# Optimization experiments

Hardware: AMD Instinct MI355X
Metric: run time of the kernel (lower is better)

Reference implementation:

```python
import jax, jax.numpy as jnp
from jax import lax
import numpy as np

B, L, E, H, R, V = 64, 512, 256, 256, 50, 20000
NEG = 1e10  # seq_max_pool mask constant


def _conv1d(x, w, b):
    # x: (B, L, Cin) -> (B, L, Cout); kernel 3, 'same' padding (pad=1)
    y = lax.conv_general_dilated(x.transpose(0, 2, 1), w, (1,), [(1, 1)],
                                 dimension_numbers=('NCH', 'OIH', 'NCH'))
    return y.transpose(0, 2, 1) + b


def _lstm_step(x, h, c, W_ih, W_hh, b_ih, b_hh):
    # single-step LSTM, PyTorch gate order (i, f, g, o)
    gates = x @ W_ih.T + b_ih + h @ W_hh.T + b_hh
    i, f, g, o = jnp.split(gates, 4, axis=-1)
    c = jax.nn.sigmoid(f) * c + jax.nn.sigmoid(i) * jnp.tanh(g)
    h = jax.nn.sigmoid(o) * jnp.tanh(c)
    return h, c


def _attention(q, ctx, W_attn, b_attn):
    # Luong attention (IBM seq2seq style). q: (B,E), ctx: (B,L,E)
    scores = jnp.einsum('be,ble->bl', q, ctx)
    attn = jax.nn.softmax(scores, axis=-1)
    mix = jnp.einsum('bl,ble->be', attn, ctx)
    return jnp.tanh(jnp.concatenate([mix, q], axis=-1) @ W_attn.T + b_attn)


def setup_inputs() -> dict:
    key = jax.random.key(0)
    ks = jax.random.split(key, 25)
    s = 0.05
    return {
        'encoder_o': jax.random.normal(ks[0], (B, L, E), jnp.float32),
        'h0': jax.random.normal(ks[1], (B, H), jnp.float32),
        'c0': jax.random.normal(ks[2], (B, H), jnp.float32),
        'sos_emb': jax.random.normal(ks[3], (E,), jnp.float32) * s,
        'rel_emb': jax.random.normal(ks[4], (R, E), jnp.float32) * s,
        'W_ih': jax.random.normal(ks[5], (4 * H, E), jnp.float32) * s,
        'W_hh': jax.random.normal(ks[6], (4 * H, H), jnp.float32) * s,
        'b_ih': jax.random.normal(ks[7], (4 * H,), jnp.float32) * s,
        'b_hh': jax.random.normal(ks[8], (4 * H,), jnp.float32) * s,
        'W_attn': jax.random.normal(ks[9], (E, 2 * E), jnp.float32) * s,
        'b_attn': jax.random.normal(ks[10], (E,), jnp.float32) * s,
        'conv_rel_w': jax.random.normal(ks[11], (E, 2 * H, 3), jnp.float32) * s,
        'conv_rel_b': jax.random.normal(ks[12], (E,), jnp.float32) * s,
        'conv_ent_w': jax.random.normal(ks[13], (E, 2 * H, 3), jnp.float32) * s,
        'conv_ent_b': jax.random.normal(ks[14], (E,), jnp.float32) * s,
        'W_rel': jax.random.normal(ks[15], (R, E), jnp.float32) * s,
        'b_rel': jax.random.normal(ks[16], (R,), jnp.float32) * s,
        'w_e1': jax.random.normal(ks[17], (E,), jnp.float32) * s,
        'b_e1': jax.random.normal(ks[18], (1,), jnp.float32) * s,
        'w_e2': jax.random.normal(ks[19], (E,), jnp.float32) * s,
        'b_e2': jax.random.normal(ks[20], (1,), jnp.float32) * s,
        'T': jax.random.randint(ks[21], (B, L), 0, V),
        'R_in': jax.random.randint(ks[22], (B,), 0, R),
        'S_K1': jax.random.randint(ks[23], (B,), 0, L),
        'S_K2': jax.random.randint(ks[24], (B,), 0, L),
    }


def reference(encoder_o, h0, c0, sos_emb, rel_emb, W_ih, W_hh, b_ih, b_hh,
              W_attn, b_attn, conv_rel_w, conv_rel_b, conv_ent_w, conv_ent_b,
              W_rel, b_rel, w_e1, b_e1, w_e2, b_e2, T, R_in, S_K1, S_K2):
    # train_forward, order=('subject','predicate','object') -> sos2ent, ent2rel, rel2ent
    # dropout is identity (eval mode)
    mask = (T > 0).astype(encoder_o.dtype)[..., None]  # (B,L,1)
    bidx = jnp.arange(B)

    def step(inp, h, c, enc, conv_w, conv_b):
        # forward_step: one LSTM step + attention over enc
        h, c = _lstm_step(inp, h, c, W_ih, W_hh, b_ih, b_hh)
        out = _attention(h, enc, W_attn, b_attn)  # (B,E)
        # seq_and_vec + permute + conv1d + permute
        cat = jnp.concatenate([enc, jnp.broadcast_to(out[:, None, :], enc.shape)], axis=-1)
        new_enc = _conv1d(cat, conv_w, conv_b)  # (B,L,E)
        a = jax.nn.gelu(new_enc, approximate=False)
        return a, new_enc, h, c

    # step 1: sos -> entity heads
    a, enc1, h, c = step(jnp.broadcast_to(sos_emb, (B, E)), h0, c0, encoder_o,
                         conv_ent_w, conv_ent_b)
    t1e1 = a @ w_e1 + b_e1  # (B,L)
    t1e2 = a @ w_e2 + b_e2

    # step 2: gathered entity span vectors -> relation logits (masked max-pool)
    inp = enc1[bidx, S_K1] + enc1[bidx, S_K2]  # seq_gather + sum, (B,E)
    a, enc2, h, c = step(inp, h, c, enc1, conv_rel_w, conv_rel_b)
    logits = a @ W_rel.T + b_rel  # (B,L,R)
    t2rel = jnp.max(logits - (1.0 - mask) * NEG, axis=1)  # seq_max_pool -> (B,R)

    # step 3: relation embedding -> entity heads
    a, enc3, h, c = step(rel_emb[R_in], h, c, enc2, conv_ent_w, conv_ent_b)
    t3e1 = a @ w_e1 + b_e1
    t3e2 = a @ w_e2 + b_e2

    return (t1e1, t1e2, t2rel, t3e1, t3e2)
```

## Files before the change

kernel.cpp:

```cpp
#include <hip/hip_runtime.h>
#include <math.h>

#define B_ 64
#define L_ 512
#define E_ 256
#define H_ 256
#define R_ 50
#define NEG_ 1.0e10f

typedef __bf16 bf16x8 __attribute__((ext_vector_type(8)));
typedef float f32x4 __attribute__((ext_vector_type(4)));

__device__ __forceinline__ float sigmoidf_(float x) { return 1.0f / (1.0f + expf(-x)); }
__device__ __forceinline__ float geluf_(float x) { return 0.5f * x * (1.0f + erff(x * 0.7071067811865476f)); }
__device__ __forceinline__ unsigned short f2bf(float x) {
    unsigned u = __float_as_uint(x);
    return (unsigned short)((u + 0x7fffu + ((u >> 16) & 1u)) >> 16);
}
__device__ __forceinline__ float bf2f(unsigned u) { return __uint_as_float(u << 16); }

__global__ void k_packs(const float* __restrict__ encoder_o, unsigned short* __restrict__ encBF0,
                        const float* __restrict__ conv_ent_w, const float* __restrict__ conv_rel_w,
                        unsigned short* __restrict__ bpE, unsigned short* __restrict__ bpR,
                        const float* __restrict__ W_rel, unsigned short* __restrict__ wpR,
// ... 25 lines not shown
        int idx = (blk - 8384) * 256 + t;
        int l = idx & 63, kc = (idx >> 6) & 7, of = idx / (8 * 64);
        int r = of * 16 + (l & 15);
        int k = kc * 32 + ((l >> 4) << 3);
        unsigned short v[8];
#pragma unroll
        for (int j = 0; j < 8; ++j) v[j] = (r < R_) ? f2bf(W_rel[(size_t)r * E_ + k + j]) : 0;
        unsigned int* dst = (unsigned int*)&wpR[(size_t)idx * 8];
#pragma unroll
        for (int j = 0; j < 4; ++j) dst[j] = (unsigned int)v[2 * j] | ((unsigned int)v[2 * j + 1] << 16);
    } else if (blk < 8904) {
        const float* w = (blk < 8648) ? conv_ent_w : conv_rel_w;
        float* wpk = (blk < 8648) ? wpkE : wpkR;
        int idx = (blk - ((blk < 8648) ? 8392 : 8648)) * 256 + t;
        int o = idx >> 8, c = idx & 255;
        const float* p = &w[(size_t)o * 1536 + 768 + c * 3];
        float w0 = p[0], w1 = p[1], w2 = p[2];
        wpk[c * 256 + o] = w0;
        wpk[65536 + c * 256 + o] = w0 + w1 + w2;
        wpk[131072 + c * 256 + o] = w2;
    } else {
        int idx = (blk - 8904) * 256 + t;
        int o = idx >> 9, k = idx & 511;
        WTat[k * 256 + o] = W_attn[idx];
    }
}

template <int MODE>
__global__ __launch_bounds__(256) void k_lstm_gemm(
    const float* __restrict__ xsrc_f, const unsigned short* __restrict__ encg,
    const int* __restrict__ i1, const int* __restrict__ i2, const int* __restrict__ rin,
    const float* __restrict__ hprev,
    const float* __restrict__ W_ih, const float* __restrict__ W_hh,
    float* __restrict__ gates) {
    const int g0 = blockIdx.x * 64;
    const int half = blockIdx.y, z = blockIdx.z;
    const int t = threadIdx.x, tx = t & 15, ty = t >> 4;
    __shared__ float Xs[64][68];
    __shared__ float Wt[64][68];
    const float* Wsrc = half ? W_hh : W_ih;
    float acc[4][4] = {{0.f}};
    for (int kb = z * 128; kb < z * 128 + 128; kb += 64) {
        __syncthreads();
#pragma unroll
        for (int i = 0; i < 4; ++i) {
            int idx = i * 256 + t;
            int row = idx >> 4, kk = (idx & 15) << 2;
            float4 xv;
            if (half) {
                xv = *(const float4*)&hprev[row * 256 + kb + kk];
            } else if (MODE == 0) {
                xv = *(const float4*)&xsrc_f[kb + kk];
            } else if (MODE == 2) {
                xv = *(const float4*)&xsrc_f[(size_t)rin[row] * 256 + kb + kk];
            } else {
                const unsigned short* p1 = &encg[((size_t)row * L_ + i1[row]) * E_ + kb + kk];
                const unsigned short* p2 = &encg[((size_t)row * L_ + i2[row]) * E_ + kb + kk];
                uint2 a = *(const uint2*)p1, b2 = *(const uint2*)p2;
                xv.x = bf2f(a.x & 0xffffu) + bf2f(b2.x & 0xffffu);
                xv.y = bf2f(a.x >> 16) + bf2f(b2.x >> 16);
                xv.z = bf2f(a.y & 0xffffu) + bf2f(b2.y & 0xffffu);
                xv.w = bf2f(a.y >> 16) + bf2f(b2.y >> 16);
            }
            *(float4*)&Xs[row][kk] = xv;
            *(float4*)&Wt[row][kk] = *(const float4*)&Wsrc[(size_t)(g0 + row) * 256 + kb + kk];
        }
        __syncthreads();
#pragma unroll
        for (int kk = 0; kk < 64; kk += 4) {
            float4 xv[4], wv[4];
#pragma unroll
            for (int i = 0; i < 4; ++i) xv[i] = *(const float4*)&Xs[ty * 4 + i][kk];
#pragma unroll
            for (int j = 0; j < 4; ++j) wv[j] = *(const float4*)&Wt[tx * 4 + j][kk];
#pragma unroll
            for (int i = 0; i < 4; ++i)
#pragma unroll
                for (int j = 0; j < 4; ++j)
                    acc[i][j] += xv[i].x * wv[j].x + xv[i].y * wv[j].y + xv[i].z * wv[j].z + xv[i].w * wv[j].w;
        }
    }
    const int seg = half * 2 + z;
#pragma unroll
    for (int i = 0; i < 4; ++i)
#pragma unroll
        for (int j = 0; j < 4; ++j)
            gates[(size_t)seg * 65536 + (size_t)(ty * 4 + i) * 1024 + g0 + tx * 4 + j] = acc[i][j];
}

__global__ __launch_bounds__(256) void k_attn_part(
    const float* __restrict__ gates, const float* __restrict__ b_ih, const float* __restrict__ b_hh,
    const float* __restrict__ c_in, float* __restrict__ c_out, float* __restrict__ h_out,
    const unsigned short* __restrict__ encbf,
    float* __restrict__ mixp, float* __restrict__ stats) {
    int b = blockIdx.y, ch = blockIdx.x, t = threadIdx.x;
    __shared__ float hs[E_];
    __shared__ float scp[64][4];
    __shared__ float sc[64];
    {
        size_t ba = (size_t)b * 1024;
        float g4[4];
#pragma unroll
        for (int g = 0; g < 4; ++g) {
            float acc = b_ih[g * 256 + t] + b_hh[g * 256 + t];
#pragma unroll
            for (int seg = 0; seg < 4; ++seg) acc += gates[(size_t)seg * 65536 + ba + g * 256 + t];
            g4[g] = acc;
        }
        float c = sigmoidf_(g4[1]) * c_in[b * H_ + t] + sigmoidf_(g4[0]) * tanhf(g4[2]);
        float hv = sigmoidf_(g4[3]) * tanhf(c);
        hs[t] = hv;
        if (ch == 0) { h_out[b * H_ + t] = hv; c_out[b * H_ + t] = c; }
    }
    __syncthreads();
    {
        int row = t >> 2, es = t & 3;
        const uint4* p = (const uint4*)&encbf[((size_t)b * L_ + ch * 64 + row) * E_ + es * 64];
        float acc = 0.f;
#pragma unroll
        for (int k = 0; k < 8; ++k) {
// ... 70 lines not shown
#pragma unroll
        for (int k2 = 0; k2 < 16; ++k2) s += red[k2][oc2][j];
        int o = oc * 64 + t;
        aout[b * E_ + o] = tanhf(s + b_attn[o]);
    }
}

__global__ __launch_bounds__(256) void k_post2(
    const float* __restrict__ aout, const float* __restrict__ wpk,
    float* __restrict__ cr0, float* __restrict__ fullv, float* __restrict__ cr2) {
    int b = blockIdx.x, m = blockIdx.y, t = threadIdx.x;
    __shared__ float os[256];
    __shared__ float red[4][64][4];
    os[t] = aout[b * E_ + t];
    __syncthreads();
    int ocol = t & 63, cs = t >> 6;
    int o4 = ocol * 4;
    const float* wp = &wpk[(size_t)m * 65536 + (size_t)(cs * 64) * 256 + o4];
    float a0 = 0.f, a1 = 0.f, a2 = 0.f, a3 = 0.f;
#pragma unroll 8
    for (int c = 0; c < 64; ++c) {
        float4 w = *(const float4*)&wp[(size_t)c * 256];
        float v = os[cs * 64 + c];
        a0 += v * w.x; a1 += v * w.y; a2 += v * w.z; a3 += v * w.w;
    }
    red[cs][ocol][0] = a0; red[cs][ocol][1] = a1; red[cs][ocol][2] = a2; red[cs][ocol][3] = a3;
    __syncthreads();
    int oc2 = t >> 2, j = t & 3;
    float s = red[0][oc2][j] + red[1][oc2][j] + red[2][oc2][j] + red[3][oc2][j];
    float* dst = (m == 0) ? cr0 : (m == 1) ? fullv : cr2;
    dst[b * E_ + t] = s;
}

template <bool FUSE_HEADS, bool WRITE_OUT>
__global__ __launch_bounds__(512, 4) void k_conv_mfma(
    const unsigned short* __restrict__ encbf, const unsigned short* __restrict__ bp,
    const float* __restrict__ bias, const float* __restrict__ fullv,
    const float* __restrict__ cr0, const float* __restrict__ cr2,
    unsigned short* __restrict__ enc_out,
    const float* __restrict__ w_e1, const float* __restrict__ b_e1,
    const float* __restrict__ w_e2, const float* __restrict__ b_e2,
    float* __restrict__ o1, float* __restrict__ o2) {
    const int b = blockIdx.y, l0 = blockIdx.x * 64;
    const int t = threadIdx.x, lane = t & 63, wid = t >> 6;
    __shared__ unsigned short As[66 * 256];
    __shared__ float hsum[2][8][64];

    for (int u = t; u < 66 * 32; u += 512) {
        int row = u >> 5, cu = u & 31;
        int l = l0 - 1 + row;
        uint4 v = {0u, 0u, 0u, 0u};
        if (l >= 0 && l < L_) v = *(const uint4*)&encbf[((size_t)b * L_ + l) * E_ + cu * 8];
        *(uint4*)&As[row * 256 + ((cu ^ (row & 7)) << 3)] = v;
    }
    __syncthreads();

    const int wo2 = wid * 2;
    f32x4 zero = {0.f, 0.f, 0.f, 0.f};
    f32x4 acc[4][2];
#pragma unroll
    for (int i = 0; i < 4; ++i) { acc[i][0] = zero; acc[i][1] = zero; }
    const int arow = lane & 15, agrp = lane >> 4;
    const unsigned short* bp0 = &bp[((size_t)wo2 * 24 * 64 + lane) * 8];
    const unsigned short* bp1 = &bp[((size_t)(wo2 + 1) * 24 * 64 + lane) * 8];

    bf16x8 bn0 = *(const bf16x8*)bp0;
    bf16x8 bn1 = *(const bf16x8*)bp1;
#pragma unroll 4
    for (int kc = 0; kc < 24; ++kc) {
        bf16x8 b0 = bn0, b1 = bn1;
        if (kc < 23) {
            bn0 = *(const bf16x8*)&bp0[(size_t)(kc + 1) * 512];
            bn1 = *(const bf16x8*)&bp1[(size_t)(kc + 1) * 512];
        }
        const int k = kc >> 3;
        const int g = ((kc & 7) << 2) + agrp;
        bf16x8 a[4];
#pragma unroll
        for (int mi = 0; mi < 4; ++mi) {
            int r = mi * 16 + arow + k;
            a[mi] = *(const bf16x8*)&As[r * 256 + ((g ^ (r & 7)) << 3)];
        }
#pragma unroll
        for (int mi = 0; mi < 4; ++mi) {
            acc[mi][0] = __builtin_amdgcn_mfma_f32_16x16x32_bf16(a[mi], b0, acc[mi][0], 0, 0, 0);
            acc[mi][1] = __builtin_amdgcn_mfma_f32_16x16x32_bf16(a[mi], b1, acc[mi][1], 0, 0, 0);
        }
    }

    float biasv[2], c0v[2], c2v[2], we1v[2], we2v[2];
#pragma unroll
    for (int ni = 0; ni < 2; ++ni) {
        int o = (wo2 + ni) * 16 + (lane & 15);
        biasv[ni] = bias[o] + fullv[b * E_ + o];
        c0v[ni] = cr0[b * E_ + o];
        c2v[ni] = cr2[b * E_ + o];
        if (FUSE_HEADS) { we1v[ni] = w_e1[o]; we2v[ni] = w_e2[o]; }
    }
    __syncthreads();

#pragma unroll
    for (int mi = 0; mi < 4; ++mi) {
#pragma unroll
        for (int r = 0; r < 4; ++r) {
            int lloc = mi * 16 + agrp * 4 + r;
            int lrow = l0 + lloc;
            float p1 = 0.f, p2 = 0.f;
#pragma unroll
            for (int ni = 0; ni < 2; ++ni) {
                float vv = acc[mi][ni][r] + biasv[ni];
                if (lrow == 0) vv -= c0v[ni];
                if (lrow == L_ - 1) vv -= c2v[ni];
                if (WRITE_OUT) As[lloc * 256 + (wo2 + ni) * 16 + (lane & 15)] = f2bf(vv);
                if (FUSE_HEADS) {
                    float gv = geluf_(vv);
                    p1 += gv * we1v[ni];
                    p2 += gv * we2v[ni];
                }
            }
            if (FUSE_HEADS) {
#pragma unroll
                for (int off = 1; off < 16; off <<= 1) {
                    p1 += __shfl_xor(p1, off);
                    p2 += __shfl_xor(p2, off);
                }
                if ((lane & 15) == 0) {
                    hsum[0][wid][lloc] = p1;
                    hsum[1][wid][lloc] = p2;
                }
            }
        }
    }
    __syncthreads();
    if (WRITE_OUT) {
        for (int u = t; u < 64 * 32; u += 512) {
            int row = u >> 5, cu = u & 31;
            *(uint4*)&enc_out[((size_t)b * L_ + l0 + row) * E_ + cu * 8] = *(const uint4*)&As[row * 256 + cu * 8];
        }
    }
    if (FUSE_HEADS && t < 128) {
        int hh = t >> 6, row = t & 63;
        float s = 0.f;
#pragma unroll
        for (int w = 0; w < 8; ++w) s += hsum[hh][w][row];
        float* dst = hh ? o2 : o1;
        const float* bb = hh ? b_e2 : b_e1;
        dst[(size_t)b * L_ + l0 + row] = s + bb[0];
    }
}

__global__ __launch_bounds__(256) void k_relmax_mfma(
    const unsigned short* __restrict__ encbf, const unsigned short* __restrict__ wp,
    const float* __restrict__ b_rel, const int* __restrict__ T,
    float* __restrict__ pmax) {
    const int b = blockIdx.y, l0 = blockIdx.x * 64;
    const int t = threadIdx.x, lane = t & 63, wid = t >> 6;
    __shared__ unsigned short As[64 * 256];
    __shared__ int Tm[64];
    __shared__ float pm[4][64];

    if (t < 64) Tm[t] = T[b * L_ + l0 + t];
    for (int u = t; u < 64 * 32; u += 256) {
        int row = u >> 5, cu = u & 31;
        uint4 q = *(const uint4*)&encbf[((size_t)b * L_ + l0 + row) * E_ + cu * 8];
        unsigned short s[8];
        unsigned qa[4] = {q.x, q.y, q.z, q.w};
#pragma unroll
        for (int j = 0; j < 4; ++j) {
            s[2 * j] = f2bf(geluf_(bf2f(qa[j] & 0xffffu)));
            s[2 * j + 1] = f2bf(geluf_(bf2f(qa[j] >> 16)));
        }
        uint4 p;
        p.x = (unsigned)s[0] | ((unsigned)s[1] << 16);
        p.y = (unsigned)s[2] | ((unsigned)s[3] << 16);
        p.z = (unsigned)s[4] | ((unsigned)s[5] << 16);
        p.w = (unsigned)s[6] | ((unsigned)s[7] << 16);
        *(uint4*)&As[row * 256 + ((cu ^ (row & 7)) << 3)] = p;
    }
    __syncthreads();

    f32x4 zero = {0.f, 0.f, 0.f, 0.f};
    f32x4 acc[4] = {zero, zero, zero, zero};
    const int arow = wid * 16 + (lane & 15);
    const int agrp = lane >> 4;
#pragma unroll 2
    for (int kc = 0; kc < 8; ++kc) {
        int g = (kc << 2) + agrp;
        bf16x8 a0 = *(const bf16x8*)&As[arow * 256 + ((g ^ (arow & 7)) << 3)];
#pragma unroll
        for (int ni = 0; ni < 4; ++ni) {
            bf16x8 bv = *(const bf16x8*)&wp[(((size_t)ni * 8 + kc) * 64 + lane) * 8];
            acc[ni] = __builtin_amdgcn_mfma_f32_16x16x32_bf16(a0, bv, acc[ni], 0, 0, 0);
        }
    }

    const int lloc_base = wid * 16 + ((lane >> 4) << 2);
#pragma unroll
    for (int ni = 0; ni < 4; ++ni) {
        int r = ni * 16 + (lane & 15);
        float brel = (r < R_) ? b_rel[r] : 0.f;
        float v = -3.0e38f;
#pragma unroll
        for (int rg = 0; rg < 4; ++rg) {
            float logit = acc[ni][rg] + brel;
            float pen = (Tm[lloc_base + rg] > 0) ? 0.f : NEG_;
            v = fmaxf(v, logit - pen);
        }
        v = fmaxf(v, __shfl_xor(v, 16));
        v = fmaxf(v, __shfl_xor(v, 32));
        if (lane < 16) pm[wid][ni * 16 + lane] = v;
    }
    __syncthreads();
    if (t < 64) {
        float m = fmaxf(fmaxf(pm[0][t], pm[1][t]), fmaxf(pm[2][t], pm[3][t]));
        pmax[((size_t)b * 8 + blockIdx.x) * 64 + t] = m;
    }
}

__global__ void k_relmax_red(const float* __restrict__ pmax, float* __restrict__ t2rel) {
    int b = blockIdx.x, r = threadIdx.x;
    if (r >= R_) return;
    float m = -3.0e38f;
    for (int ch = 0; ch < 8; ++ch) m = fmaxf(m, pmax[((size_t)b * 8 + ch) * 64 + r]);
    t2rel[b * R_ + r] = m;
}

extern "C" void kernel_launch(void* const* d_in, const int* in_sizes, int n_in,
                              void* d_out, int out_size, void* d_ws, size_t ws_size,
                              hipStream_t stream) {
    const float* encoder_o = (const float*)d_in[0];
    const float* h0 = (const float*)d_in[1];
    const float* c0 = (const float*)d_in[2];
    const float* sos_emb = (const float*)d_in[3];
    const float* rel_emb = (const float*)d_in[4];
    const float* W_ih = (const float*)d_in[5];
    const float* W_hh = (const float*)d_in[6];
    const float* b_ih = (const float*)d_in[7];
    const float* b_hh = (const float*)d_in[8];
    const float* W_attn = (const float*)d_in[9];
    const float* b_attn = (const float*)d_in[10];
    const float* conv_rel_w = (const float*)d_in[11];
    const float* conv_rel_b = (const float*)d_in[12];
    const float* conv_ent_w = (const float*)d_in[13];
    const float* conv_ent_b = (const float*)d_in[14];
    const float* W_rel = (const float*)d_in[15];
    const float* b_rel = (const float*)d_in[16];
    const float* w_e1 = (const float*)d_in[17];
    const float* b_e1 = (const float*)d_in[18];
    const float* w_e2 = (const float*)d_in[19];
    const float* b_e2 = (const float*)d_in[20];
    const int* T = (const int*)d_in[21];
    const int* R_in = (const int*)d_in[22];
    const int* S_K1 = (const int*)d_in[23];
    const int* S_K2 = (const int*)d_in[24];

    float* out = (float*)d_out;
    float* t1e1 = out;
    float* t1e2 = out + 32768;
    float* t2rel = out + 65536;
    float* t3e1 = out + 68736;
    float* t3e2 = out + 101504;

    float* ws = (float*)d_ws;
    size_t off = 0;
    unsigned short* encBF0 = (unsigned short*)(ws + off); off += (size_t)B_ * L_ * E_ / 2;
    unsigned short* encA = (unsigned short*)(ws + off); off += (size_t)B_ * L_ * E_ / 2;
    unsigned short* encB = (unsigned short*)(ws + off); off += (size_t)B_ * L_ * E_ / 2;
    float* gates = ws + off; off += 4 * 65536;
    float* hbuf = ws + off; off += B_ * H_;
    float* cb1 = ws + off; off += B_ * H_;
    float* cb2 = ws + off; off += B_ * H_;
    float* cb3 = ws + off; off += B_ * H_;
    float* mixp = ws + off; off += (size_t)B_ * 8 * E_;
    float* stats = ws + off; off += B_ * 8 * 2;
    float* aoutb = ws + off; off += B_ * E_;
    float* fullv = ws + off; off += B_ * E_;
    float* cr0 = ws + off; off += B_ * E_;
    float* cr2 = ws + off; off += B_ * E_;
    float* pmax = ws + off; off += B_ * 8 * 64;
    float* wpkE = ws + off; off += 3 * 65536;
    float* wpkR = ws + off; off += 3 * 65536;
    float* WTat = ws + off; off += 131072;
    unsigned short* bpE = (unsigned short*)(ws + off); off += 16 * 24 * 64 * 8 / 2;
    unsigned short* bpR = (unsigned short*)(ws + off); off += 16 * 24 * 64 * 8 / 2;
    unsigned short* wpR = (unsigned short*)(ws + off); off += 4 * 8 * 64 * 8 / 2;

    dim3 convGrid(8, B_);
    dim3 attnGrid(8, B_);
    dim3 rmGrid(8, B_);
    dim3 lstmGrid(16, 2, 2);
    dim3 p1Grid(B_, 4);
    dim3 p2Grid(B_, 3);

    k_packs<<<9416, 256, 0, stream>>>(encoder_o, encBF0, conv_ent_w, conv_rel_w,
                                      bpE, bpR, W_rel, wpR, wpkE, wpkR, W_attn, WTat);

    k_lstm_gemm<0><<<lstmGrid, 256, 0, stream>>>(sos_emb, nullptr, nullptr, nullptr, nullptr,
                                                 h0, W_ih, W_hh, gates);
    k_attn_part<<<attnGrid, 256, 0, stream>>>(gates, b_ih, b_hh, c0, cb1, hbuf, encBF0, mixp, stats);
    k_post1<<<p1Grid, 256, 0, stream>>>(mixp, stats, hbuf, WTat, b_attn, aoutb);
    k_post2<<<p2Grid, 256, 0, stream>>>(aoutb, wpkE, cr0, fullv, cr2);
    k_conv_mfma<true, true><<<convGrid, 512, 0, stream>>>(encBF0, bpE, conv_ent_b, fullv, cr0, cr2,
                                                          encA, w_e1, b_e1, w_e2, b_e2, t1e1, t1e2);

    k_lstm_gemm<1><<<lstmGrid, 256, 0, stream>>>(nullptr, encA, S_K1, S_K2, nullptr,
                                                 hbuf, W_ih, W_hh, gates);
    k_attn_part<<<attnGrid, 256, 0, stream>>>(gates, b_ih, b_hh, cb1, cb2, hbuf, encA, mixp, stats);
    k_post1<<<p1Grid, 256, 0, stream>>>(mixp, stats, hbuf, WTat, b_attn, aoutb);
    k_post2<<<p2Grid, 256, 0, stream>>>(aoutb, wpkR, cr0, fullv, cr2);
    k_conv_mfma<false, true><<<convGrid, 512, 0, stream>>>(encA, bpR, conv_rel_b, fullv, cr0, cr2,
                                                           encB, nullptr, nullptr, nullptr, nullptr,
                                                           nullptr, nullptr);
    k_relmax_mfma<<<rmGrid, 256, 0, stream>>>(encB, wpR, b_rel, T, pmax);
    k_relmax_red<<<B_, 64, 0, stream>>>(pmax, t2rel);

    k_lstm_gemm<2><<<lstmGrid, 256, 0, stream>>>(rel_emb, nullptr, nullptr, nullptr, R_in,
                                                 hbuf, W_ih, W_hh, gates);
    k_attn_part<<<attnGrid, 256, 0, stream>>>(gates, b_ih, b_hh, cb2, cb3, hbuf, encB, mixp, stats);
    k_post1<<<p1Grid, 256, 0, stream>>>(mixp, stats, hbuf, WTat, b_attn, aoutb);
    k_post2<<<p2Grid, 256, 0, stream>>>(aoutb, wpkE, cr0, fullv, cr2);
    k_conv_mfma<true, false><<<convGrid, 512, 0, stream>>>(encB, bpE, conv_ent_b, fullv, cr0, cr2,
                                                           nullptr, w_e1, b_e1, w_e2, b_e2, t3e1, t3e2);
}
```

Before: 190.5 us.

## Fuse relation-logit max-pool into conv kernel and widen conv blocks to 1024 threads

```diff
diff --git a/kernel.cpp b/kernel.cpp
--- a/kernel.cpp
+++ b/kernel.cpp
@@ -271,21 +271,28 @@
     dst[b * E_ + t] = s;
 }
 
-template <bool FUSE_HEADS, bool WRITE_OUT>
-__global__ __launch_bounds__(512, 4) void k_conv_mfma(
+template <bool FUSE_HEADS, bool WRITE_OUT, bool FUSE_REL>
+__global__ __launch_bounds__(1024, 8) void k_conv_mfma(
     const unsigned short* __restrict__ encbf, const unsigned short* __restrict__ bp,
     const float* __restrict__ bias, const float* __restrict__ fullv,
     const float* __restrict__ cr0, const float* __restrict__ cr2,
     unsigned short* __restrict__ enc_out,
     const float* __restrict__ w_e1, const float* __restrict__ b_e1,
     const float* __restrict__ w_e2, const float* __restrict__ b_e2,
-    float* __restrict__ o1, float* __restrict__ o2) {
+    float* __restrict__ o1, float* __restrict__ o2,
+    const unsigned short* __restrict__ wprel, const float* __restrict__ b_rel,
+    const int* __restrict__ T, float* __restrict__ pmax) {
     const int b = blockIdx.y, l0 = blockIdx.x * 64;
     const int t = threadIdx.x, lane = t & 63, wid = t >> 6;
     __shared__ unsigned short As[66 * 256];
-    __shared__ float hsum[2][8][64];
-
-    for (int u = t; u < 66 * 32; u += 512) {
+    __shared__ float hsum[2][FUSE_HEADS ? 16 : 1][FUSE_HEADS ? 64 : 1];
+    __shared__ unsigned short G[FUSE_REL ? 64 * 256 : 64];
+    __shared__ float pm[FUSE_REL ? 16 : 1][16];
+    __shared__ int Tm[64];
+
+    if (FUSE_REL && t < 64) Tm[t] = T[b * L_ + l0 + t];
+
+    for (int u = t; u < 66 * 32; u += 1024) {
         int row = u >> 5, cu = u & 31;
         int l = l0 - 1 + row;
         uint4 v = {0u, 0u, 0u, 0u};
@@ -294,48 +301,32 @@
     }
     __syncthreads();
 
-    const int wo2 = wid * 2;
+    const int of = wid;
     f32x4 zero = {0.f, 0.f, 0.f, 0.f};
-    f32x4 acc[4][2];
-#pragma unroll
-    for (int i = 0; i < 4; ++i) { acc[i][0] = zero; acc[i][1] = zero; }
+    f32x4 acc[4] = {zero, zero, zero, zero};
     const int arow = lane & 15, agrp = lane >> 4;
-    const unsigned short* bp0 = &bp[((size_t)wo2 * 24 * 64 + lane) * 8];
-    const unsigned short* bp1 = &bp[((size_t)(wo2 + 1) * 24 * 64 + lane) * 8];
-
-    bf16x8 bn0 = *(const bf16x8*)bp0;
-    bf16x8 bn1 = *(const bf16x8*)bp1;
+    const unsigned short* bp0 = &bp[((size_t)of * 24 * 64 + lane) * 8];
+
+    bf16x8 bn = *(const bf16x8*)bp0;
 #pragma unroll 4
     for (int kc = 0; kc < 24; ++kc) {
-        bf16x8 b0 = bn0, b1 = bn1;
-        if (kc < 23) {
-            bn0 = *(const bf16x8*)&bp0[(size_t)(kc + 1) * 512];
-            bn1 = *(const bf16x8*)&bp1[(size_t)(kc + 1) * 512];
-        }
+        bf16x8 bcur = bn;
+        if (kc < 23) bn = *(const bf16x8*)&bp0[(size_t)(kc + 1) * 512];
         const int k = kc >> 3;
         const int g = ((kc & 7) << 2) + agrp;
-        bf16x8 a[4];
 #pragma unroll
         for (int mi = 0; mi < 4; ++mi) {
             int r = mi * 16 + arow + k;
-            a[mi] = *(const bf16x8*)&As[r * 256 + ((g ^ (r & 7)) << 3)];
-        }
-#pragma unroll
-        for (int mi = 0; mi < 4; ++mi) {
-            acc[mi][0] = __builtin_amdgcn_mfma_f32_16x16x32_bf16(a[mi], b0, acc[mi][0], 0, 0, 0);
-            acc[mi][1] = __builtin_amdgcn_mfma_f32_16x16x32_bf16(a[mi], b1, acc[mi][1], 0, 0, 0);
-        }
-    }
-
-    float biasv[2], c0v[2], c2v[2], we1v[2], we2v[2];
-#pragma unroll
-    for (int ni = 0; ni < 2; ++ni) {
-        int o = (wo2 + ni) * 16 + (lane & 15);
-        biasv[ni] = bias[o] + fullv[b * E_ + o];
-        c0v[ni] = cr0[b * E_ + o];
-        c2v[ni] = cr2[b * E_ + o];
-        if (FUSE_HEADS) { we1v[ni] = w_e1[o]; we2v[ni] = w_e2[o]; }
-    }
+            bf16x8 a = *(const bf16x8*)&As[r * 256 + ((g ^ (r & 7)) << 3)];
+            acc[mi] = __builtin_amdgcn_mfma_f32_16x16x32_bf16(a, bcur, acc[mi], 0, 0, 0);
+        }
+    }
+
+    const int o = of * 16 + (lane & 15);
+    const float biasv = bias[o] + fullv[b * E_ + o];
+    const float c0v = cr0[b * E_ + o], c2v = cr2[b * E_ + o];
+    float we1v = 0.f, we2v = 0.f;
+    if (FUSE_HEADS) { we1v = w_e1[o]; we2v = w_e2[o]; }
     __syncthreads();
 
 #pragma unroll
@@ -344,20 +335,15 @@
         for (int r = 0; r < 4; ++r) {
             int lloc = mi * 16 + agrp * 4 + r;
             int lrow = l0 + lloc;
-            float p1 = 0.f, p2 = 0.f;
-#pragma unroll
-            for (int ni = 0; ni < 2; ++ni) {
-                float vv = acc[mi][ni][r] + biasv[ni];
-                if (lrow == 0) vv -= c0v[ni];
-                if (lrow == L_ - 1) vv -= c2v[ni];
-                if (WRITE_OUT) As[lloc * 256 + (wo2 + ni) * 16 + (lane & 15)] = f2bf(vv);
-                if (FUSE_HEADS) {
-                    float gv = geluf_(vv);
-                    p1 += gv * we1v[ni];
-                    p2 += gv * we2v[ni];
-                }
-            }
+            float vv = acc[mi][r] + biasv;
+            if (lrow == 0) vv -= c0v;
+            if (lrow == L_ - 1) vv -= c2v;
+            int swz = (((o >> 3) ^ (lloc & 7)) << 3) + (o & 7);
+            if (WRITE_OUT) As[lloc * 256 + swz] = f2bf(vv);
+            if (FUSE_REL) G[lloc * 256 + swz] = f2bf(geluf_(vv));
             if (FUSE_HEADS) {
+                float gv = geluf_(vv);
+                float p1 = gv * we1v, p2 = gv * we2v;
 #pragma unroll
                 for (int off = 1; off < 16; off <<= 1) {
                     p1 += __shfl_xor(p1, off);
@@ -371,88 +357,53 @@
         }
     }
     __syncthreads();
+
     if (WRITE_OUT) {
-        for (int u = t; u < 64 * 32; u += 512) {
+        for (int u = t; u < 64 * 32; u += 1024) {
             int row = u >> 5, cu = u & 31;
-            *(uint4*)&enc_out[((size_t)b * L_ + l0 + row) * E_ + cu * 8] = *(const uint4*)&As[row * 256 + cu * 8];
+            *(uint4*)&enc_out[((size_t)b * L_ + l0 + row) * E_ + cu * 8] =
+                *(const uint4*)&As[row * 256 + ((cu ^ (row & 7)) << 3)];
         }
     }
     if (FUSE_HEADS && t < 128) {
         int hh = t >> 6, row = t & 63;
         float s = 0.f;
 #pragma unroll
-        for (int w = 0; w < 8; ++w) s += hsum[hh][w][row];
+        for (int w = 0; w < 16; ++w) s += hsum[hh][w][row];
         float* dst = hh ? o2 : o1;
         const float* bb = hh ? b_e2 : b_e1;
         dst[(size_t)b * L_ + l0 + row] = s + bb[0];
     }
-}
-
-__global__ __launch_bounds__(256) void k_relmax_mfma(
-    const unsigned short* __restrict__ encbf, const unsigned short* __restrict__ wp,
-    const float* __restrict__ b_rel, const int* __restrict__ T,
-    float* __restrict__ pmax) {
-    const int b = blockIdx.y, l0 = blockIdx.x * 64;
-    const int t = threadIdx.x, lane = t & 63, wid = t >> 6;
-    __shared__ unsigned short As[64 * 256];
-    __shared__ int Tm[64];
-    __shared__ float pm[4][64];
-
-    if (t < 64) Tm[t] = T[b * L_ + l0 + t];
-    for (int u = t; u < 64 * 32; u += 256) {
-        int row = u >> 5, cu = u & 31;
-        uint4 q = *(const uint4*)&encbf[((size_t)b * L_ + l0 + row) * E_ + cu * 8];
-        unsigned short s[8];
-        unsigned qa[4] = {q.x, q.y, q.z, q.w};
-#pragma unroll
-        for (int j = 0; j < 4; ++j) {
-            s[2 * j] = f2bf(geluf_(bf2f(qa[j] & 0xffffu)));
-            s[2 * j + 1] = f2bf(geluf_(bf2f(qa[j] >> 16)));
-        }
-        uint4 p;
-        p.x = (unsigned)s[0] | ((unsigned)s[1] << 16);
-        p.y = (unsigned)s[2] | ((unsigned)s[3] << 16);
-        p.z = (unsigned)s[4] | ((unsigned)s[5] << 16);
-        p.w = (unsigned)s[6] | ((unsigned)s[7] << 16);
-        *(uint4*)&As[row * 256 + ((cu ^ (row & 7)) << 3)] = p;
-    }
-    __syncthreads();
-
-    f32x4 zero = {0.f, 0.f, 0.f, 0.f};
-    f32x4 acc[4] = {zero, zero, zero, zero};
-    const int arow = wid * 16 + (lane & 15);
-    const int agrp = lane >> 4;
+    if (FUSE_REL) {
+        const int mi = wid & 3, nj = wid >> 2;
+        f32x4 accr = zero;
+        const int ar = mi * 16 + (lane & 15);
 #pragma unroll 2
-    for (int kc = 0; kc < 8; ++kc) {
-        int g = (kc << 2) + agrp;
-        bf16x8 a0 = *(const bf16x8*)&As[arow * 256 + ((g ^ (arow & 7)) << 3)];
-#pragma unroll
-        for (int ni = 0; ni < 4; ++ni) {
-            bf16x8 bv = *(const bf16x8*)&wp[(((size_t)ni * 8 + kc) * 64 + lane) * 8];
-            acc[ni] = __builtin_amdgcn_mfma_f32_16x16x32_bf16(a0, bv, acc[ni], 0, 0, 0);
-        }
-    }
-
-    const int lloc_base = wid * 16 + ((lane >> 4) << 2);
-#pragma unroll
-    for (int ni = 0; ni < 4; ++ni) {
-        int r = ni * 16 + (lane & 15);
-        float brel = (r < R_) ? b_rel[r] : 0.f;
+        for (int kc = 0; kc < 8; ++kc) {
+            int g = (kc << 2) + agrp;
+            bf16x8 a = *(const bf16x8*)&G[ar * 256 + ((g ^ (ar & 7)) << 3)];
+            bf16x8 bv = *(const bf16x8*)&wprel[(((size_t)nj * 8 + kc) * 64 + lane) * 8];
+            accr = __builtin_amdgcn_mfma_f32_16x16x32_bf16(a, bv, accr, 0, 0, 0);
+        }
+        int rr = nj * 16 + (lane & 15);
+        float brel = (rr < R_) ? b_rel[rr] : 0.f;
         float v = -3.0e38f;
 #pragma unroll
         for (int rg = 0; rg < 4; ++rg) {
-            float logit = acc[ni][rg] + brel;
-            float pen = (Tm[lloc_base + rg] > 0) ? 0.f : NEG_;
+            float logit = accr[rg] + brel;
+            float pen = (Tm[mi * 16 + agrp * 4 + rg] > 0) ? 0.f : NEG_;
             v = fmaxf(v, logit - pen);
         }
         v = fmaxf(v, __shfl_xor(v, 16));
         v = fmaxf(v, __shfl_xor(v, 32));
-        if (lane < 16) pm[wid][ni * 16 + lane] = v;
-    }
-    __syncthreads();
-    if (t < 64) {
-        float m = fmaxf(fmaxf(pm[0][t], pm[1][t]), fmaxf(pm[2][t], pm[3][t]));
-        pmax[((size_t)b * 8 + blockIdx.x) * 64 + t] = m;
+        if (lane < 16) pm[wid][lane] = v;
+        __syncthreads();
+        if (t < 64) {
+            int nj2 = t >> 4, rl = t & 15;
+            float m = fmaxf(fmaxf(pm[nj2 * 4 + 0][rl], pm[nj2 * 4 + 1][rl]),
+                            fmaxf(pm[nj2 * 4 + 2][rl], pm[nj2 * 4 + 3][rl]));
+            pmax[((size_t)b * 8 + blockIdx.x) * 64 + nj2 * 16 + rl] = m;
+        }
     }
 }
 
@@ -526,7 +477,6 @@
 
     dim3 convGrid(8, B_);
     dim3 attnGrid(8, B_);
-    dim3 rmGrid(8, B_);
     dim3 lstmGrid(16, 2, 2);
     dim3 p1Grid(B_, 4);
     dim3 p2Grid(B_, 3);
@@ -539,18 +489,18 @@
     k_attn_part<<<attnGrid, 256, 0, stream>>>(gates, b_ih, b_hh, c0, cb1, hbuf, encBF0, mixp, stats);
     k_post1<<<p1Grid, 256, 0, stream>>>(mixp, stats, hbuf, WTat, b_attn, aoutb);
     k_post2<<<p2Grid, 256, 0, stream>>>(aoutb, wpkE, cr0, fullv, cr2);
-    k_conv_mfma<true, true><<<convGrid, 512, 0, stream>>>(encBF0, bpE, conv_ent_b, fullv, cr0, cr2,
-                                                          encA, w_e1, b_e1, w_e2, b_e2, t1e1, t1e2);
+    k_conv_mfma<true, true, false><<<convGrid, 1024, 0, stream>>>(
+        encBF0, bpE, conv_ent_b, fullv, cr0, cr2, encA,
+        w_e1, b_e1, w_e2, b_e2, t1e1, t1e2, nullptr, nullptr, nullptr, nullptr);
 
     k_lstm_gemm<1><<<lstmGrid, 256, 0, stream>>>(nullptr, encA, S_K1, S_K2, nullptr,
                                                  hbuf, W_ih, W_hh, gates);
     k_attn_part<<<attnGrid, 256, 0, stream>>>(gates, b_ih, b_hh, cb1, cb2, hbuf, encA, mixp, stats);
     k_post1<<<p1Grid, 256, 0, stream>>>(mixp, stats, hbuf, WTat, b_attn, aoutb);
     k_post2<<<p2Grid, 256, 0, stream>>>(aoutb, wpkR, cr0, fullv, cr2);
-    k_conv_mfma<false, true><<<convGrid, 512, 0, stream>>>(encA, bpR, conv_rel_b, fullv, cr0, cr2,
-                                                           encB, nullptr, nullptr, nullptr, nullptr,
-                                                           nullptr, nullptr);
-    k_relmax_mfma<<<rmGrid, 256, 0, stream>>>(encB, wpR, b_rel, T, pmax);
+    k_conv_mfma<false, true, true><<<convGrid, 1024, 0, stream>>>(
+        encA, bpR, conv_rel_b, fullv, cr0, cr2, encB,
+        nullptr, nullptr, nullptr, nullptr, nullptr, nullptr, wpR, b_rel, T, pmax);
     k_relmax_red<<<B_, 64, 0, stream>>>(pmax, t2rel);
 
     k_lstm_gemm<2><<<lstmGrid, 256, 0, stream>>>(rel_emb, nullptr, nullptr, nullptr, R_in,
@@ -558,6 +508,7 @@
     k_attn_part<<<attnGrid, 256, 0, stream>>>(gates, b_ih, b_hh, cb2, cb3, hbuf, encB, mixp, stats);
     k_post1<<<p1Grid, 256, 0, stream>>>(mixp, stats, hbuf, WTat, b_attn, aoutb);
     k_post2<<<p2Grid, 256, 0, stream>>>(aoutb, wpkE, cr0, fullv, cr2);
-    k_conv_mfma<true, false><<<convGrid, 512, 0, stream>>>(encB, bpE, conv_ent_b, fullv, cr0, cr2,
-                                                           nullptr, w_e1, b_e1, w_e2, b_e2, t3e1, t3e2);
-}
+    k_conv_mfma<true, false, false><<<convGrid, 1024, 0, stream>>>(
+        encB, bpE, conv_ent_b, fullv, cr0, cr2, nullptr,
+        w_e1, b_e1, w_e2, b_e2, t3e1, t3e2, nullptr, nullptr, nullptr, nullptr);
+}
```

Result: slower. 197.6 us (+3.7%).

## Enlarge conv MFMA tile to 128 rows with 4x4 per-wave output blocks

Applied to the files above, without the earlier changes.

```diff
diff --git a/kernel.cpp b/kernel.cpp
--- a/kernel.cpp
+++ b/kernel.cpp
@@ -280,12 +280,12 @@
     const float* __restrict__ w_e1, const float* __restrict__ b_e1,
     const float* __restrict__ w_e2, const float* __restrict__ b_e2,
     float* __restrict__ o1, float* __restrict__ o2) {
-    const int b = blockIdx.y, l0 = blockIdx.x * 64;
+    const int b = blockIdx.y, l0 = blockIdx.x * 128;
     const int t = threadIdx.x, lane = t & 63, wid = t >> 6;
-    __shared__ unsigned short As[66 * 256];
-    __shared__ float hsum[2][8][64];
-
-    for (int u = t; u < 66 * 32; u += 512) {
+    __shared__ unsigned short As[130 * 256];
+    __shared__ float hsum[2][4][128];
+
+    for (int u = t; u < 130 * 32; u += 512) {
         int row = u >> 5, cu = u & 31;
         int l = l0 - 1 + row;
         uint4 v = {0u, 0u, 0u, 0u};
@@ -294,46 +294,41 @@
     }
     __syncthreads();
 
-    const int wo2 = wid * 2;
+    const int og = wid & 3, lg = wid >> 2;
     f32x4 zero = {0.f, 0.f, 0.f, 0.f};
-    f32x4 acc[4][2];
-#pragma unroll
-    for (int i = 0; i < 4; ++i) { acc[i][0] = zero; acc[i][1] = zero; }
+    f32x4 acc[4][4];
+#pragma unroll
+    for (int i = 0; i < 4; ++i)
+#pragma unroll
+        for (int j = 0; j < 4; ++j) acc[i][j] = zero;
     const int arow = lane & 15, agrp = lane >> 4;
-    const unsigned short* bp0 = &bp[((size_t)wo2 * 24 * 64 + lane) * 8];
-    const unsigned short* bp1 = &bp[((size_t)(wo2 + 1) * 24 * 64 + lane) * 8];
-
-    bf16x8 bn0 = *(const bf16x8*)bp0;
-    bf16x8 bn1 = *(const bf16x8*)bp1;
-#pragma unroll 4
+    const int rbase = lg * 64 + arow;
+
+#pragma unroll 2
     for (int kc = 0; kc < 24; ++kc) {
-        bf16x8 b0 = bn0, b1 = bn1;
-        if (kc < 23) {
-            bn0 = *(const bf16x8*)&bp0[(size_t)(kc + 1) * 512];
-            bn1 = *(const bf16x8*)&bp1[(size_t)(kc + 1) * 512];
-        }
         const int k = kc >> 3;
         const int g = ((kc & 7) << 2) + agrp;
-        bf16x8 a[4];
+        bf16x8 a[4], bv[4];
 #pragma unroll
         for (int mi = 0; mi < 4; ++mi) {
-            int r = mi * 16 + arow + k;
+            int r = rbase + mi * 16 + k;
             a[mi] = *(const bf16x8*)&As[r * 256 + ((g ^ (r & 7)) << 3)];
         }
 #pragma unroll
-        for (int mi = 0; mi < 4; ++mi) {
-            acc[mi][0] = __builtin_amdgcn_mfma_f32_16x16x32_bf16(a[mi], b0, acc[mi][0], 0, 0, 0);
-            acc[mi][1] = __builtin_amdgcn_mfma_f32_16x16x32_bf16(a[mi], b1, acc[mi][1], 0, 0, 0);
-        }
-    }
-
-    float biasv[2], c0v[2], c2v[2], we1v[2], we2v[2];
-#pragma unroll
-    for (int ni = 0; ni < 2; ++ni) {
-        int o = (wo2 + ni) * 16 + (lane & 15);
+        for (int ni = 0; ni < 4; ++ni)
+            bv[ni] = *(const bf16x8*)&bp[(((size_t)(og * 4 + ni) * 24 + kc) * 64 + lane) * 8];
+#pragma unroll
+        for (int mi = 0; mi < 4; ++mi)
+#pragma unroll
+            for (int ni = 0; ni < 4; ++ni)
+                acc[mi][ni] = __builtin_amdgcn_mfma_f32_16x16x32_bf16(a[mi], bv[ni], acc[mi][ni], 0, 0, 0);
+    }
+
+    float biasv[4], we1v[4], we2v[4];
+#pragma unroll
+    for (int ni = 0; ni < 4; ++ni) {
+        int o = (og * 4 + ni) * 16 + (lane & 15);
         biasv[ni] = bias[o] + fullv[b * E_ + o];
-        c0v[ni] = cr0[b * E_ + o];
-        c2v[ni] = cr2[b * E_ + o];
         if (FUSE_HEADS) { we1v[ni] = w_e1[o]; we2v[ni] = w_e2[o]; }
     }
     __syncthreads();
@@ -342,15 +337,16 @@
     for (int mi = 0; mi < 4; ++mi) {
 #pragma unroll
         for (int r = 0; r < 4; ++r) {
-            int lloc = mi * 16 + agrp * 4 + r;
+            int lloc = lg * 64 + mi * 16 + agrp * 4 + r;
             int lrow = l0 + lloc;
             float p1 = 0.f, p2 = 0.f;
 #pragma unroll
-            for (int ni = 0; ni < 2; ++ni) {
+            for (int ni = 0; ni < 4; ++ni) {
+                int o = (og * 4 + ni) * 16 + (lane & 15);
                 float vv = acc[mi][ni][r] + biasv[ni];
-                if (lrow == 0) vv -= c0v[ni];
-                if (lrow == L_ - 1) vv -= c2v[ni];
-                if (WRITE_OUT) As[lloc * 256 + (wo2 + ni) * 16 + (lane & 15)] = f2bf(vv);
+                if (lrow == 0) vv -= cr0[b * E_ + o];
+                if (lrow == L_ - 1) vv -= cr2[b * E_ + o];
+                if (WRITE_OUT) As[lloc * 256 + o] = f2bf(vv);
                 if (FUSE_HEADS) {
                     float gv = geluf_(vv);
                     p1 += gv * we1v[ni];
@@ -364,24 +360,23 @@
                     p2 += __shfl_xor(p2, off);
                 }
                 if ((lane & 15) == 0) {
-                    hsum[0][wid][lloc] = p1;
-                    hsum[1][wid][lloc] = p2;
+                    hsum[0][og][lloc] = p1;
+                    hsum[1][og][lloc] = p2;
                 }
             }
         }
     }
     __syncthreads();
+
     if (WRITE_OUT) {
-        for (int u = t; u < 64 * 32; u += 512) {
+        for (int u = t; u < 128 * 32; u += 512) {
             int row = u >> 5, cu = u & 31;
             *(uint4*)&enc_out[((size_t)b * L_ + l0 + row) * E_ + cu * 8] = *(const uint4*)&As[row * 256 + cu * 8];
         }
     }
-    if (FUSE_HEADS && t < 128) {
-        int hh = t >> 6, row = t & 63;
-        float s = 0.f;
-#pragma unroll
-        for (int w = 0; w < 8; ++w) s += hsum[hh][w][row];
+    if (FUSE_HEADS && t < 256) {
+        int hh = t >> 7, row = t & 127;
+        float s = hsum[hh][0][row] + hsum[hh][1][row] + hsum[hh][2][row] + hsum[hh][3][row];
         float* dst = hh ? o2 : o1;
         const float* bb = hh ? b_e2 : b_e1;
         dst[(size_t)b * L_ + l0 + row] = s + bb[0];
@@ -524,7 +519,7 @@
     unsigned short* bpR = (unsigned short*)(ws + off); off += 16 * 24 * 64 * 8 / 2;
     unsigned short* wpR = (unsigned short*)(ws + off); off += 4 * 8 * 64 * 8 / 2;
 
-    dim3 convGrid(8, B_);
+    dim3 convGrid(4, B_);
     dim3 attnGrid(8, B_);
     dim3 rmGrid(8, B_);
     dim3 lstmGrid(16, 2, 2);
```

Result: slower. 215.7 us (+13.2%).

## Fuse relation max-pool into conv kernel and software-pipeline LDS A-fragment loads

Applied to the files above, without the earlier changes.

```diff
diff --git a/kernel.cpp b/kernel.cpp
--- a/kernel.cpp
+++ b/kernel.cpp
@@ -81,7 +81,8 @@
     const int* __restrict__ i1, const int* __restrict__ i2, const int* __restrict__ rin,
     const float* __restrict__ hprev,
     const float* __restrict__ W_ih, const float* __restrict__ W_hh,
-    float* __restrict__ gates) {
+    float* __restrict__ gates,
+    const float* __restrict__ pmax, float* __restrict__ t2rel) {
     const int g0 = blockIdx.x * 64;
     const int half = blockIdx.y, z = blockIdx.z;
     const int t = threadIdx.x, tx = t & 15, ty = t >> 4;
@@ -135,6 +136,18 @@
 #pragma unroll
         for (int j = 0; j < 4; ++j)
             gates[(size_t)seg * 65536 + (size_t)(ty * 4 + i) * 1024 + g0 + tx * 4 + j] = acc[i][j];
+
+    if (MODE == 2 && blockIdx.x == 0 && half == 0 && z == 0) {
+        for (int i = t; i < B_ * 64; i += 256) {
+            int b = i >> 6, r = i & 63;
+            if (r < R_) {
+                float m = -3.0e38f;
+#pragma unroll
+                for (int ch = 0; ch < 8; ++ch) m = fmaxf(m, pmax[((size_t)b * 8 + ch) * 64 + r]);
+                t2rel[b * R_ + r] = m;
+            }
+        }
+    }
 }
 
 __global__ __launch_bounds__(256) void k_attn_part(
@@ -271,7 +284,7 @@
     dst[b * E_ + t] = s;
 }
 
-template <bool FUSE_HEADS, bool WRITE_OUT>
+template <bool FUSE_HEADS, bool WRITE_OUT, bool FUSE_REL>
 __global__ __launch_bounds__(512, 4) void k_conv_mfma(
     const unsigned short* __restrict__ encbf, const unsigned short* __restrict__ bp,
     const float* __restrict__ bias, const float* __restrict__ fullv,
@@ -279,11 +292,17 @@
     unsigned short* __restrict__ enc_out,
     const float* __restrict__ w_e1, const float* __restrict__ b_e1,
     const float* __restrict__ w_e2, const float* __restrict__ b_e2,
-    float* __restrict__ o1, float* __restrict__ o2) {
+    float* __restrict__ o1, float* __restrict__ o2,
+    const unsigned short* __restrict__ wprel, const float* __restrict__ b_rel,
+    const int* __restrict__ T, float* __restrict__ pmax) {
     const int b = blockIdx.y, l0 = blockIdx.x * 64;
     const int t = threadIdx.x, lane = t & 63, wid = t >> 6;
     __shared__ unsigned short As[66 * 256];
-    __shared__ float hsum[2][8][64];
+    __shared__ float hsum[2][FUSE_HEADS ? 8 : 1][FUSE_HEADS ? 64 : 1];
+    __shared__ float pm[FUSE_REL ? 8 : 1][2][16];
+    __shared__ int Tm[FUSE_REL ? 64 : 1];
+
+    if (FUSE_REL && t < 64) Tm[t] = T[b * L_ + l0 + t];
 
     for (int u = t; u < 66 * 32; u += 512) {
         int row = u >> 5, cu = u & 31;
@@ -303,27 +322,36 @@
     const unsigned short* bp0 = &bp[((size_t)wo2 * 24 * 64 + lane) * 8];
     const unsigned short* bp1 = &bp[((size_t)(wo2 + 1) * 24 * 64 + lane) * 8];
 
-    bf16x8 bn0 = *(const bf16x8*)bp0;
-    bf16x8 bn1 = *(const bf16x8*)bp1;
+    bf16x8 bc0 = *(const bf16x8*)bp0;
+    bf16x8 bc1 = *(const bf16x8*)bp1;
+    bf16x8 a[4];
+#pragma unroll
+    for (int mi = 0; mi < 4; ++mi) {
+        int r = mi * 16 + arow;
+        a[mi] = *(const bf16x8*)&As[r * 256 + ((agrp ^ (r & 7)) << 3)];
+    }
 #pragma unroll 4
     for (int kc = 0; kc < 24; ++kc) {
-        bf16x8 b0 = bn0, b1 = bn1;
+        bf16x8 bn0, bn1, an[4];
         if (kc < 23) {
             bn0 = *(const bf16x8*)&bp0[(size_t)(kc + 1) * 512];
             bn1 = *(const bf16x8*)&bp1[(size_t)(kc + 1) * 512];
-        }
-        const int k = kc >> 3;
-        const int g = ((kc & 7) << 2) + agrp;
-        bf16x8 a[4];
+            const int kn = (kc + 1) >> 3;
+            const int gn = (((kc + 1) & 7) << 2) + agrp;
+#pragma unroll
+            for (int mi = 0; mi < 4; ++mi) {
+                int r = mi * 16 + arow + kn;
+                an[mi] = *(const bf16x8*)&As[r * 256 + ((gn ^ (r & 7)) << 3)];
+            }
+        }
 #pragma unroll
         for (int mi = 0; mi < 4; ++mi) {
-            int r = mi * 16 + arow + k;
-            a[mi] = *(const bf16x8*)&As[r * 256 + ((g ^ (r & 7)) << 3)];
-        }
-#pragma unroll
-        for (int mi = 0; mi < 4; ++mi) {
-            acc[mi][0] = __builtin_amdgcn_mfma_f32_16x16x32_bf16(a[mi], b0, acc[mi][0], 0, 0, 0);
-            acc[mi][1] = __builtin_amdgcn_mfma_f32_16x16x32_bf16(a[mi], b1, acc[mi][1], 0, 0, 0);
+            acc[mi][0] = __builtin_amdgcn_mfma_f32_16x16x32_bf16(a[mi], bc0, acc[mi][0], 0, 0, 0);
+            acc[mi][1] = __builtin_amdgcn_mfma_f32_16x16x32_bf16(a[mi], bc1, acc[mi][1], 0, 0, 0);
+        }
+        if (kc < 23) {
+            bc0 = bn0; bc1 = bn1;
+            a[0] = an[0]; a[1] = an[1]; a[2] = an[2]; a[3] = an[3];
         }
     }
 
@@ -347,10 +375,15 @@
             float p1 = 0.f, p2 = 0.f;
 #pragma unroll
             for (int ni = 0; ni < 2; ++ni) {
+                int o = (wo2 + ni) * 16 + (lane & 15);
                 float vv = acc[mi][ni][r] + biasv[ni];
                 if (lrow == 0) vv -= c0v[ni];
                 if (lrow == L_ - 1) vv -= c2v[ni];
-                if (WRITE_OUT) As[lloc * 256 + (wo2 + ni) * 16 + (lane & 15)] = f2bf(vv);
+                if (WRITE_OUT || FUSE_REL) {
+                    int idx = FUSE_REL ? (lloc * 256 + ((((o >> 3) ^ (lloc & 7))) << 3) + (o & 7))
+                                       : (lloc * 256 + o);
+                    As[idx] = f2bf(vv);
+                }
                 if (FUSE_HEADS) {
                     float gv = geluf_(vv);
                     p1 += gv * we1v[ni];
@@ -371,10 +404,24 @@
         }
     }
     __syncthreads();
+
     if (WRITE_OUT) {
         for (int u = t; u < 64 * 32; u += 512) {
             int row = u >> 5, cu = u & 31;
-            *(uint4*)&enc_out[((size_t)b * L_ + l0 + row) * E_ + cu * 8] = *(const uint4*)&As[row * 256 + cu * 8];
+            int src = FUSE_REL ? (row * 256 + ((cu ^ (row & 7)) << 3)) : (row * 256 + cu * 8);
+            uint4 q = *(const uint4*)&As[src];
+            *(uint4*)&enc_out[((size_t)b * L_ + l0 + row) * E_ + cu * 8] = q;
+            if (FUSE_REL) {
+                unsigned qa[4] = {q.x, q.y, q.z, q.w};
+#pragma unroll
+                for (int j = 0; j < 4; ++j) {
+                    unsigned lo = f2bf(geluf_(bf2f(qa[j] & 0xffffu)));
+                    unsigned hi = f2bf(geluf_(bf2f(qa[j] >> 16)));
+                    qa[j] = lo | (hi << 16);
+                }
+                uint4 gq = {qa[0], qa[1], qa[2], qa[3]};
+                *(uint4*)&As[src] = gq;
+            }
         }
     }
     if (FUSE_HEADS && t < 128) {
@@ -386,82 +433,47 @@
         const float* bb = hh ? b_e2 : b_e1;
         dst[(size_t)b * L_ + l0 + row] = s + bb[0];
     }
-}
-
-__global__ __launch_bounds__(256) void k_relmax_mfma(
-    const unsigned short* __restrict__ encbf, const unsigned short* __restrict__ wp,
-    const float* __restrict__ b_rel, const int* __restrict__ T,
-    float* __restrict__ pmax) {
-    const int b = blockIdx.y, l0 = blockIdx.x * 64;
-    const int t = threadIdx.x, lane = t & 63, wid = t >> 6;
-    __shared__ unsigned short As[64 * 256];
-    __shared__ int Tm[64];
-    __shared__ float pm[4][64];
-
-    if (t < 64) Tm[t] = T[b * L_ + l0 + t];
-    for (int u = t; u < 64 * 32; u += 256) {
-        int row = u >> 5, cu = u & 31;
-        uint4 q = *(const uint4*)&encbf[((size_t)b * L_ + l0 + row) * E_ + cu * 8];
-        unsigned short s[8];
-        unsigned qa[4] = {q.x, q.y, q.z, q.w};
-#pragma unroll
-        for (int j = 0; j < 4; ++j) {
-            s[2 * j] = f2bf(geluf_(bf2f(qa[j] & 0xffffu)));
-            s[2 * j + 1] = f2bf(geluf_(bf2f(qa[j] >> 16)));
-        }
-        uint4 p;
-        p.x = (unsigned)s[0] | ((unsigned)s[1] << 16);
-        p.y = (unsigned)s[2] | ((unsigned)s[3] << 16);
-        p.z = (unsigned)s[4] | ((unsigned)s[5] << 16);
-        p.w = (unsigned)s[6] | ((unsigned)s[7] << 16);
-        *(uint4*)&As[row * 256 + ((cu ^ (row & 7)) << 3)] = p;
-    }
-    __syncthreads();
-
-    f32x4 zero = {0.f, 0.f, 0.f, 0.f};
-    f32x4 acc[4] = {zero, zero, zero, zero};
-    const int arow = wid * 16 + (lane & 15);
-    const int agrp = lane >> 4;
+    if (FUSE_REL) {
+        __syncthreads();
+        const int mi = wid & 3, njp = wid >> 2;
+        f32x4 accr[2] = {zero, zero};
+        const int ar = mi * 16 + arow;
 #pragma unroll 2
-    for (int kc = 0; kc < 8; ++kc) {
-        int g = (kc << 2) + agrp;
-        bf16x8 a0 = *(const bf16x8*)&As[arow * 256 + ((g ^ (arow & 7)) << 3)];
-#pragma unroll
-        for (int ni = 0; ni < 4; ++ni) {
-            bf16x8 bv = *(const bf16x8*)&wp[(((size_t)ni * 8 + kc) * 64 + lane) * 8];
-            acc[ni] = __builtin_amdgcn_mfma_f32_16x16x32_bf16(a0, bv, acc[ni], 0, 0, 0);
-        }
-    }
-
-    const int lloc_base = wid * 16 + ((lane >> 4) << 2);
-#pragma unroll
-    for (int ni = 0; ni < 4; ++ni) {
-        int r = ni * 16 + (lane & 15);
-        float brel = (r < R_) ? b_rel[r] : 0.f;
-        float v = -3.0e38f;
-#pragma unroll
-        for (int rg = 0; rg < 4; ++rg) {
-            float logit = acc[ni][rg] + brel;
-            float pen = (Tm[lloc_base + rg] > 0) ? 0.f : NEG_;
-            v = fmaxf(v, logit - pen);
-        }
-        v = fmaxf(v, __shfl_xor(v, 16));
-        v = fmaxf(v, __shfl_xor(v, 32));
-        if (lane < 16) pm[wid][ni * 16 + lane] = v;
-    }
-    __syncthreads();
-    if (t < 64) {
-        float m = fmaxf(fmaxf(pm[0][t], pm[1][t]), fmaxf(pm[2][t], pm[3][t]));
-        pmax[((size_t)b * 8 + blockIdx.x) * 64 + t] = m;
-    }
-}
-
-__global__ void k_relmax_red(const float* __restrict__ pmax, float* __restrict__ t2rel) {
-    int b = blockIdx.x, r = threadIdx.x;
-    if (r >= R_) return;
-    float m = -3.0e38f;
-    for (int ch = 0; ch < 8; ++ch) m = fmaxf(m, pmax[((size_t)b * 8 + ch) * 64 + r]);
-    t2rel[b * R_ + r] = m;
+        for (int kc = 0; kc < 8; ++kc) {
+            int g = (kc << 2) + agrp;
+            bf16x8 av = *(const bf16x8*)&As[ar * 256 + ((g ^ (ar & 7)) << 3)];
+#pragma unroll
+            for (int q = 0; q < 2; ++q) {
+                int nj = njp * 2 + q;
+                bf16x8 bv = *(const bf16x8*)&wprel[(((size_t)nj * 8 + kc) * 64 + lane) * 8];
+                accr[q] = __builtin_amdgcn_mfma_f32_16x16x32_bf16(av, bv, accr[q], 0, 0, 0);
+            }
+        }
+#pragma unroll
+        for (int q = 0; q < 2; ++q) {
+            int nj = njp * 2 + q;
+            int rr = nj * 16 + (lane & 15);
+            float brel = (rr < R_) ? b_rel[rr] : 0.f;
+            float v = -3.0e38f;
+#pragma unroll
+            for (int rg = 0; rg < 4; ++rg) {
+                int lloc = mi * 16 + agrp * 4 + rg;
+                float pen = (Tm[lloc] > 0) ? 0.f : NEG_;
+                v = fmaxf(v, accr[q][rg] + brel - pen);
+            }
+            v = fmaxf(v, __shfl_xor(v, 16));
+            v = fmaxf(v, __shfl_xor(v, 32));
+            if (lane < 16) pm[wid][q][lane] = v;
+        }
+        __syncthreads();
+        if (t < 64) {
+            int nj = t >> 4, rl = t & 15;
+            int q = nj & 1, wb = (nj >> 1) * 4;
+            float m = fmaxf(fmaxf(pm[wb][q][rl], pm[wb + 1][q][rl]),
+                            fmaxf(pm[wb + 2][q][rl], pm[wb + 3][q][rl]));
+            pmax[((size_t)b * 8 + blockIdx.x) * 64 + t] = m;
+        }
+    }
 }
 
 extern "C" void kernel_launch(void* const* d_in, const int* in_sizes, int n_in,
@@ -526,7 +538,6 @@
 
     dim3 convGrid(8, B_);
     dim3 attnGrid(8, B_);
-    dim3 rmGrid(8, B_);
     dim3 lstmGrid(16, 2, 2);
     dim3 p1Grid(B_, 4);
     dim3 p2Grid(B_, 3);
@@ -535,29 +546,29 @@
                                       bpE, bpR, W_rel, wpR, wpkE, wpkR, W_attn, WTat);
 
     k_lstm_gemm<0><<<lstmGrid, 256, 0, stream>>>(sos_emb, nullptr, nullptr, nullptr, nullptr,
-                                                 h0, W_ih, W_hh, gates);
+                                                 h0, W_ih, W_hh, gates, nullptr, nullptr);
     k_attn_part<<<attnGrid, 256, 0, stream>>>(gates, b_ih, b_hh, c0, cb1, hbuf, encBF0, mixp, stats);
     k_post1<<<p1Grid, 256, 0, stream>>>(mixp, stats, hbuf, WTat, b_attn, aoutb);
     k_post2<<<p2Grid, 256, 0, stream>>>(aoutb, wpkE, cr0, fullv, cr2);
-    k_conv_mfma<true, true><<<convGrid, 512, 0, stream>>>(encBF0, bpE, conv_ent_b, fullv, cr0, cr2,
-                                                          encA, w_e1, b_e1, w_e2, b_e2, t1e1, t1e2);
+    k_conv_mfma<true, true, false><<<convGrid, 512, 0, stream>>>(
+        encBF0, bpE, conv_ent_b, fullv, cr0, cr2, encA,
+        w_e1, b_e1, w_e2, b_e2, t1e1, t1e2, nullptr, nullptr, nullptr, nullptr);
 
     k_lstm_gemm<1><<<lstmGrid, 256, 0, stream>>>(nullptr, encA, S_K1, S_K2, nullptr,
-                                                 hbuf, W_ih, W_hh, gates);
+                                                 hbuf, W_ih, W_hh, gates, nullptr, nullptr);
     k_attn_part<<<attnGrid, 256, 0, stream>>>(gates, b_ih, b_hh, cb1, cb2, hbuf, encA, mixp, stats);
     k_post1<<<p1Grid, 256, 0, stream>>>(mixp, stats, hbuf, WTat, b_attn, aoutb);
     k_post2<<<p2Grid, 256, 0, stream>>>(aoutb, wpkR, cr0, fullv, cr2);
-    k_conv_mfma<false, true><<<convGrid, 512, 0, stream>>>(encA, bpR, conv_rel_b, fullv, cr0, cr2,
-                                                           encB, nullptr, nullptr, nullptr, nullptr,
-                                                           nullptr, nullptr);
-    k_relmax_mfma<<<rmGrid, 256, 0, stream>>>(encB, wpR, b_rel, T, pmax);
-    k_relmax_red<<<B_, 64, 0, stream>>>(pmax, t2rel);
+    k_conv_mfma<false, true, true><<<convGrid, 512, 0, stream>>>(
+        encA, bpR, conv_rel_b, fullv, cr0, cr2, encB,
+        nullptr, nullptr, nullptr, nullptr, nullptr, nullptr, wpR, b_rel, T, pmax);
 
     k_lstm_gemm<2><<<lstmGrid, 256, 0, stream>>>(rel_emb, nullptr, nullptr, nullptr, R_in,
-                                                 hbuf, W_ih, W_hh, gates);
+                                                 hbuf, W_ih, W_hh, gates, pmax, t2rel);
     k_attn_part<<<attnGrid, 256, 0, stream>>>(gates, b_ih, b_hh, cb2, cb3, hbuf, encB, mixp, stats);
     k_post1<<<p1Grid, 256, 0, stream>>>(mixp, stats, hbuf, WTat, b_attn, aoutb);
     k_post2<<<p2Grid, 256, 0, stream>>>(aoutb, wpkE, cr0, fullv, cr2);
-    k_conv_mfma<true, false><<<convGrid, 512, 0, stream>>>(encB, bpE, conv_ent_b, fullv, cr0, cr2,
-                                                           nullptr, w_e1, b_e1, w_e2, b_e2, t3e1, t3e2);
-}
+    k_conv_mfma<true, false, false><<<convGrid, 512, 0, stream>>>(
+        encB, bpE, conv_ent_b, fullv, cr0, cr2, nullptr,
+        w_e1, b_e1, w_e2, b_e2, t3e1, t3e2, nullptr, nullptr, nullptr, nullptr);
+}
```

Result: no change. 189.8 us (-0.4%).
